# Optimization experiments

Measured on AMD Instinct MI355X. Metric: run time of the kernel, lower is better.

The kernel has to match this reference:

```python
import jax, jax.numpy as jnp
import numpy as np

B, S, E = 256, 512, 512
H = 512            # hidden_dim[0]
SUB = 512          # subreddit_embedding
TFIDF = 799
HDIMS = [256, 128] # hidden_dim[1:]


def _lin(key, fan_in, fan_out):
    kw, kb = jax.random.split(key)
    s = 1.0 / np.sqrt(fan_in)
    w = jax.random.uniform(kw, (fan_in, fan_out), jnp.float32, -s, s)
    b = jax.random.uniform(kb, (fan_out,), jnp.float32, -s, s)
    return w, b


def setup_inputs() -> dict:
    key = jax.random.key(0)
    ks = jax.random.split(key, 12)
    x = jax.random.normal(ks[0], (B, S, E), jnp.float32)
    ts = jax.random.uniform(ks[1], (B, S), jnp.float32)
    tfidf = jax.random.uniform(ks[2], (B, TFIDF), jnp.float32)
    W_all_w, W_all_b = _lin(ks[3], H, 4 * H)
    U_all_w, U_all_b = _lin(ks[4], E, 4 * H)
    W_d_w, W_d_b = _lin(ks[5], H, H)
    fc_tfidf_w, fc_tfidf_b = _lin(ks[6], TFIDF, SUB)
    l1_w, l1_b = _lin(ks[7], H + SUB, HDIMS[0])
    l2_w, l2_b = _lin(ks[8], HDIMS[0], HDIMS[1])
    lo_w, lo_b = _lin(ks[9], HDIMS[1], 2)
    return dict(historic_features=x, timestamp=ts, tf_idf_vector=tfidf,
                W_all_w=W_all_w, W_all_b=W_all_b, U_all_w=U_all_w, U_all_b=U_all_b,
                W_d_w=W_d_w, W_d_b=W_d_b, fc_tfidf_w=fc_tfidf_w, fc_tfidf_b=fc_tfidf_b,
                l1_w=l1_w, l1_b=l1_b, l2_w=l2_w, l2_b=l2_b, lo_w=lo_w, lo_b=lo_b)


def _time_lstm(x, ts, W_all_w, W_all_b, U_all_w, U_all_b, W_d_w, W_d_b):
    # Precompute input projections for all steps at once: [B,S,4H]
    u_all = jnp.einsum('bse,eh->bsh', x, U_all_w) + U_all_b

    def step(carry, xs):
        h, c = carry
        u_t, t_t = xs  # [B,4H], [B]
        c_s1 = jnp.tanh(c @ W_d_w + W_d_b)
        c_adj = (c - c_s1) + c_s1 * t_t[:, None]
        outs = h @ W_all_w + W_all_b + u_t
        f, i, o, c_tmp = jnp.split(jax.nn.sigmoid(outs), 4, axis=1)
        c_new = f * c_adj + i * c_tmp
        h_new = o * jnp.tanh(c_new)
        return (h_new, c_new), h_new

    h0 = jnp.zeros((x.shape[0], H), x.dtype)
    c0 = jnp.zeros((x.shape[0], H), x.dtype)
    (_, _), hs = jax.lax.scan(step, (h0, c0),
                              (jnp.swapaxes(u_all, 0, 1), jnp.swapaxes(ts, 0, 1)))
    return jnp.swapaxes(hs, 0, 1)  # [B,S,H]


def reference(historic_features, timestamp, tf_idf_vector,
              W_all_w, W_all_b, U_all_w, U_all_b, W_d_w, W_d_b,
              fc_tfidf_w, fc_tfidf_b, l1_w, l1_b, l2_w, l2_b, lo_w, lo_b):
    outputs = _time_lstm(historic_features, timestamp,
                         W_all_w, W_all_b, U_all_w, U_all_b, W_d_w, W_d_b)
    outputs = jnp.mean(outputs, axis=1)  # [B,H]
    sub = jax.nn.relu(tf_idf_vector @ fc_tfidf_w + fc_tfidf_b)  # [B,SUB]
    x = jnp.concatenate([sub, outputs], axis=1)  # [B, SUB+H]
    # dropout is identity in eval mode
    x = jax.nn.relu(x @ l1_w + l1_b)
    x = jax.nn.relu(x @ l2_w + l2_b)
    return x @ lo_w + lo_b  # [B,2]
```

## Files before the change

kernel.cpp:

```cpp
#include <hip/hip_runtime.h>
#include <hip/hip_cooperative_groups.h>

namespace cg = cooperative_groups;

#define BB 256
#define SS 512
#define EE 512
#define HH 512
#define G4 2048
#define NTF 799

typedef __attribute__((ext_vector_type(8))) short bf16x8;
typedef __attribute__((ext_vector_type(4))) float f32x4;

__device__ __forceinline__ float my_sig(float v) { return 1.0f / (1.0f + __expf(-v)); }
__device__ __forceinline__ float my_tanh(float v) { float e = __expf(2.0f * v); return 1.0f - 2.0f / (e + 1.0f); }

__device__ __forceinline__ unsigned short f2bf(float f) {
    unsigned u = __builtin_bit_cast(unsigned, f);
    u = (u + 0x7FFFu + ((u >> 16) & 1u)) >> 16;
    return (unsigned short)u;
}
__device__ __forceinline__ float bf2f(unsigned short h) {
    unsigned u = ((unsigned)h) << 16;
    return __builtin_bit_cast(float, u);
}
__device__ __forceinline__ unsigned packsplit(float f) {
    unsigned short hi = f2bf(f);
    unsigned short lo = f2bf(f - bf2f(hi));
    return ((unsigned)hi << 16) | (unsigned)lo;
}
__device__ __forceinline__ bf16x8 unhi(uint4 a, uint4 b) {
    union { unsigned u[4]; bf16x8 v; } r;
    r.u[0] = __builtin_amdgcn_perm(a.y, a.x, 0x07060302u);
    r.u[1] = __builtin_amdgcn_perm(a.w, a.z, 0x07060302u);
    r.u[2] = __builtin_amdgcn_perm(b.y, b.x, 0x07060302u);
    r.u[3] = __builtin_amdgcn_perm(b.w, b.z, 0x07060302u);
    return r.v;
}
__device__ __forceinline__ bf16x8 unlo(uint4 a, uint4 b) {
    union { unsigned u[4]; bf16x8 v; } r;
    r.u[0] = __builtin_amdgcn_perm(a.y, a.x, 0x05040100u);
    r.u[1] = __builtin_amdgcn_perm(a.w, a.z, 0x05040100u);
    r.u[2] = __builtin_amdgcn_perm(b.y, b.x, 0x05040100u);
    r.u[3] = __builtin_amdgcn_perm(b.w, b.z, 0x05040100u);
    return r.v;
}

__device__ __forceinline__ void ld4_sc1(uint4& d, const unsigned* p) {
    asm volatile("global_load_dwordx4 %0, %1, off sc0 sc1" : "=v"(d) : "v"(p));
}
__device__ __forceinline__ void ld4_nt(uint4& d, const uint4* p) {
    asm volatile("global_load_dwordx4 %0, %1, off nt" : "=v"(d) : "v"(p));
}
__device__ __forceinline__ void st_devu(unsigned* p, unsigned v) {
    __hip_atomic_store(p, v, __ATOMIC_RELAXED, __HIP_MEMORY_SCOPE_AGENT);
}
__device__ __forceinline__ unsigned ld_devu(const unsigned* p) {
    return __hip_atomic_load(p, __ATOMIC_RELAXED, __HIP_MEMORY_SCOPE_AGENT);
}

__global__ void __launch_bounds__(256)
prep_split(const float* __restrict__ Wall, const float* __restrict__ Uall,
           const float* __restrict__ Wd,
           unsigned short* __restrict__ B1, unsigned short* __restrict__ B2)
{
    const int t = blockIdx.x * 256 + threadIdx.x;
    if (t < 262144) {
        const int lane = t & 63, wc = (t >> 6) & 3, kc = (t >> 8) & 31, cgi = t >> 13;
        const int kb = ((kc & 15) << 5) + ((lane >> 4) << 3);
        const int col = (wc << 9) + (cgi << 4) + (lane & 15);
        const float* src = (kc < 16) ? Wall : Uall;
        bf16x8 vh, vl;
#pragma unroll
        for (int j = 0; j < 8; ++j) {
            float f = src[(size_t)(kb + j) * G4 + col];
            unsigned short h16 = f2bf(f);
            vh[j] = (short)h16;
            vl[j] = (short)f2bf(f - bf2f(h16));
        }
        const int g = t >> 6;
        *(bf16x8*)(B1 + ((size_t)(g * 2 + 0) * 64 + lane) * 8) = vh;
        *(bf16x8*)(B1 + ((size_t)(g * 2 + 1) * 64 + lane) * 8) = vl;
    } else if (t < 262144 + 32768) {
        const int u = t - 262144;
        const int lane = u & 63, kch = (u >> 6) & 15, cgi = u >> 10;
        const int kb = (kch << 5) + ((lane >> 4) << 3);
        const int col = (cgi << 4) + (lane & 15);
        bf16x8 vh, vl;
#pragma unroll
        for (int j = 0; j < 8; ++j) {
            float f = Wd[(size_t)(kb + j) * HH + col];
            unsigned short h16 = f2bf(f);
            vh[j] = (short)h16;
            vl[j] = (short)f2bf(f - bf2f(h16));
        }
        const int g = u >> 6;
        *(bf16x8*)(B2 + ((size_t)(g * 2 + 0) * 64 + lane) * 8) = vh;
        *(bf16x8*)(B2 + ((size_t)(g * 2 + 1) * 64 + lane) * 8) = vl;
    }
}

__global__ void __launch_bounds__(256)
prep_pack(const float* __restrict__ x, unsigned* __restrict__ xp)
{
    const size_t i = (size_t)blockIdx.x * 256 + threadIdx.x;
    float4 v = ((const float4*)x)[i];
    uint4 p;
    p.x = packsplit(v.x); p.y = packsplit(v.y);
    p.z = packsplit(v.z); p.w = packsplit(v.w);
    ((uint4*)xp)[i] = p;
}

#define B1FRAG(kcv, wcv, term) (*(const bf16x8*)(B1 +                          \
    ((size_t)(((cgi * 32 + (kcv)) * 4 + (wcv)) * 2 + (term)) * 64 + lane) * 8))
#define B2FRAG(kchv, term) (*(const bf16x8*)(B2 +                              \
    ((size_t)((cgi * 16 + (kchv)) * 2 + (term)) * 64 + lane) * 8))

#define GPIDX(row, slot, col)                                                  \
    ((row) * 256 + (slot) * 64 + ((col) ^ (((((row) & 3) ^ (((row) >> 2) & 3))) << 4)))

__global__ void __launch_bounds__(512) __attribute__((amdgpu_waves_per_eu(2)))
lstm_persistent(const float* __restrict__ x, const unsigned* __restrict__ xp,
                const int use_xp, const float* __restrict__ ts,
                const float* __restrict__ ball, const float* __restrict__ bu,
                const float* __restrict__ bd,
                const unsigned short* __restrict__ B1,
                const unsigned short* __restrict__ B2,
                unsigned* __restrict__ h2a, unsigned* __restrict__ h2b,
                unsigned* __restrict__ c2a, unsigned* __restrict__ c2b,
                float* __restrict__ hsum, float* __restrict__ tsT,
                unsigned* __restrict__ barv)
{
    cg::grid_group grid = cg::this_grid();
    const int tid = threadIdx.x;
    const int bid = blockIdx.x;
    const int gtid = (bid << 9) + tid;

    for (int i = gtid; i < BB * HH; i += 131072) { h2a[i] = 0u; c2a[i] = 0u; }
    for (int i = gtid; i < BB * SS; i += 131072) {
        int b = i >> 9, s = i & 511;
        tsT[s * BB + b] = ts[i];
    }
    if (gtid < 1024) barv[gtid] = 0u;
    grid.sync();

    const int xcd = bid & 7, tt = bid >> 3;
    const int cgi = (xcd << 2) | (tt & 3);
    const int rg  = tt >> 2;
    const int r0  = rg << 5;
    const int m0  = cgi << 4;

    const int wid = tid >> 6, lane = tid & 63;
    const int lrow = lane & 15, lk8 = lane >> 4;
    const int kq = wid & 3, ch = wid >> 2;
    const int srow = tid >> 4, scb = tid & 15;
    const int rl = srow, mj = scb;

    __shared__ __align__(16) unsigned R1[32 * 512];
    __shared__ __align__(16) unsigned R2[32 * 512];
    uint4* R1v = (uint4*)R1;
    uint4* R2v = (uint4*)R2;
    float* gp  = (float*)R2;
    float* gp2 = (float*)(R2 + 8192);

    unsigned* arr = barv;
    const int myline = rg << 6;

    bf16x8 wfh[4][2], wfl[4][2], d2h[2], d2l[2];
#pragma unroll
    for (int q = 0; q < 4; ++q)
#pragma unroll
        for (int wcl = 0; wcl < 2; ++wcl) {
            wfh[q][wcl] = B1FRAG((kq << 2) + q, (ch << 1) + wcl, 0);
            wfl[q][wcl] = B1FRAG((kq << 2) + q, (ch << 1) + wcl, 1);
        }
#pragma unroll
    for (int e = 0; e < 2; ++e) {
        d2h[e] = B2FRAG((wid << 1) + e, 0);
        d2l[e] = B2FRAG((wid << 1) + e, 1);
    }

    float bias4[4];
#pragma unroll
    for (int k = 0; k < 4; ++k)
        bias4[k] = ball[(k << 9) + m0 + mj] + bu[(k << 9) + m0 + mj];
    const float bias2v = bd[m0 + mj];

    float creg = 0.f, hsreg = 0.f;

#pragma unroll 1
    for (int s = 0; s < SS; ++s) {
        const unsigned* h2p = (s & 1) ? h2b : h2a;
        const unsigned* c2p = (s & 1) ? c2b : c2a;
        unsigned* h2n = (s & 1) ? h2a : h2b;
        unsigned* c2n = (s & 1) ? c2a : c2b;

        __syncthreads();
        if (use_xp) {
            const uint4* xpp = (const uint4*)(xp + (size_t)(r0 + srow) * (SS * EE)
                                              + (size_t)s * EE);
            uint4 xv[8];
#pragma unroll
            for (int j = 0; j < 8; ++j) ld4_nt(xv[j], xpp + (scb + (j << 4)));
            asm volatile("s_waitcnt vmcnt(0)" ::: "memory");
            __builtin_amdgcn_sched_barrier(0);
#pragma unroll
            for (int j = 0; j < 8; ++j) {
                const int ci = scb + (j << 4);
                R1v[srow * 128 + (ci ^ (srow & 7))] = xv[j];
            }
        } else {
            const float* xfp = x + (size_t)(r0 + srow) * (SS * EE) + (size_t)s * EE;
#pragma unroll
            for (int j = 0; j < 8; ++j) {
                const int ci = scb + (j << 4);
                float4 v = *(const float4*)(xfp + (ci << 2));
                uint4 pk;
                pk.x = packsplit(v.x); pk.y = packsplit(v.y);
                pk.z = packsplit(v.z); pk.w = packsplit(v.w);
                R1v[srow * 128 + (ci ^ (srow & 7))] = pk;
            }
        }
        __syncthreads();

        f32x4 acc[2][2];
        acc[0][0] = acc[0][1] = acc[1][0] = acc[1][1] = (f32x4){0.f, 0.f, 0.f, 0.f};
        {
            bf16x8 ufh[2][2], ufl[2][2];
#pragma unroll
            for (int wcl = 0; wcl < 2; ++wcl) {
                ufh[0][wcl] = B1FRAG(16 + (kq << 2), (ch << 1) + wcl, 0);
                ufl[0][wcl] = B1FRAG(16 + (kq << 2), (ch << 1) + wcl, 1);
            }
#pragma unroll
            for (int q = 0; q < 4; ++q) {
                const int cur = q & 1, nxt = cur ^ 1;
                if (q < 3) {
#pragma unroll
                    for (int wcl = 0; wcl < 2; ++wcl) {
                        ufh[nxt][wcl] = B1FRAG(16 + (kq << 2) + q + 1, (ch << 1) + wcl, 0);
                        ufl[nxt][wcl] = B1FRAG(16 + (kq << 2) + q + 1, (ch << 1) + wcl, 1);
                    }
                }
                const int kcp = (kq << 2) + q;
#pragma unroll
                for (int wr = 0; wr < 2; ++wr) {
                    const int row_ = (wr << 4) | lrow;
                    const int cb_  = (kcp << 3) + (lk8 << 1);
                    uint4 qa = R1v[row_ * 128 + (cb_ ^ (row_ & 7))];
                    uint4 qb = R1v[row_ * 128 + ((cb_ + 1) ^ (row_ & 7))];
                    bf16x8 ah = unhi(qa, qb), al = unlo(qa, qb);
#pragma unroll
                    for (int wcl = 0; wcl < 2; ++wcl) {
                        acc[wr][wcl] = __builtin_amdgcn_mfma_f32_16x16x32_bf16(ah, ufh[cur][wcl], acc[wr][wcl], 0, 0, 0);
                        acc[wr][wcl] = __builtin_amdgcn_mfma_f32_16x16x32_bf16(ah, ufl[cur][wcl], acc[wr][wcl], 0, 0, 0);
                        acc[wr][wcl] = __builtin_amdgcn_mfma_f32_16x16x32_bf16(al, ufh[cur][wcl], acc[wr][wcl], 0, 0, 0);
                    }
                }
            }
        }

        if (tid == 0) {
            const unsigned tgt = 32u * (unsigned)s;
            while (ld_devu(&arr[myline]) < tgt)
                __builtin_amdgcn_s_sleep(4);
        }
        __syncthreads();
        asm volatile("" ::: "memory");

        {
            const unsigned* hp = h2p + (r0 + srow) * HH;
            const unsigned* cp = c2p + (r0 + srow) * HH;
            uint4 hv[8], cv[8];
#pragma unroll
            for (int j = 0; j < 8; ++j) ld4_sc1(hv[j], hp + ((scb + (j << 4)) << 2));
#pragma unroll
            for (int j = 0; j < 8; ++j) ld4_sc1(cv[j], cp + ((scb + (j << 4)) << 2));
            asm volatile("s_waitcnt vmcnt(8)" ::: "memory");
            __builtin_amdgcn_sched_barrier(0);
#pragma unroll
            for (int j = 0; j < 8; ++j) {
                const int ci = scb + (j << 4);
                R2v[srow * 128 + (ci ^ (srow & 7))] = hv[j];
            }
            asm volatile("s_waitcnt vmcnt(0)" ::: "memory");
            __builtin_amdgcn_sched_barrier(0);
#pragma unroll
            for (int j = 0; j < 8; ++j) {
                const int ci = scb + (j << 4);
                R1v[srow * 128 + (ci ^ (srow & 7))] = cv[j];
            }
        }
        __syncthreads();

#pragma unroll
        for (int q = 0; q < 4; ++q) {
            const int kcp = (kq << 2) + q;
#pragma unroll
            for (int wr = 0; wr < 2; ++wr) {
                const int row_ = (wr << 4) | lrow;
                const int cb_  = (kcp << 3) + (lk8 << 1);
                uint4 qa = R2v[row_ * 128 + (cb_ ^ (row_ & 7))];
                uint4 qb = R2v[row_ * 128 + ((cb_ + 1) ^ (row_ & 7))];
                bf16x8 ah = unhi(qa, qb), al = unlo(qa, qb);
#pragma unroll
                for (int wcl = 0; wcl < 2; ++wcl) {
                    acc[wr][wcl] = __builtin_amdgcn_mfma_f32_16x16x32_bf16(ah, wfh[q][wcl], acc[wr][wcl], 0, 0, 0);
                    acc[wr][wcl] = __builtin_amdgcn_mfma_f32_16x16x32_bf16(ah, wfl[q][wcl], acc[wr][wcl], 0, 0, 0);
                    acc[wr][wcl] = __builtin_amdgcn_mfma_f32_16x16x32_bf16(al, wfh[q][wcl], acc[wr][wcl], 0, 0, 0);
                }
            }
        }
        f32x4 acc2[2];
        acc2[0] = (f32x4){0.f, 0.f, 0.f, 0.f};
        acc2[1] = (f32x4){0.f, 0.f, 0.f, 0.f};
#pragma unroll
        for (int e = 0; e < 2; ++e) {
            const int kch = (wid << 1) + e;
#pragma unroll
            for (int wr = 0; wr < 2; ++wr) {
                const int row_ = (wr << 4) | lrow;
                const int cb_  = (kch << 3) + (lk8 << 1);
                uint4 qa = R1v[row_ * 128 + (cb_ ^ (row_ & 7))];
                uint4 qb = R1v[row_ * 128 + ((cb_ + 1) ^ (row_ & 7))];
                bf16x8 ah = unhi(qa, qb), al = unlo(qa, qb);
                acc2[wr] = __builtin_amdgcn_mfma_f32_16x16x32_bf16(ah, d2h[e], acc2[wr], 0, 0, 0);
                acc2[wr] = __builtin_amdgcn_mfma_f32_16x16x32_bf16(ah, d2l[e], acc2[wr], 0, 0, 0);
                acc2[wr] = __builtin_amdgcn_mfma_f32_16x16x32_bf16(al, d2h[e], acc2[wr], 0, 0, 0);
            }
        }
        __syncthreads();

#pragma unroll
        for (int wr = 0; wr < 2; ++wr)
#pragma unroll
            for (int wcl = 0; wcl < 2; ++wcl)
#pragma unroll
                for (int i = 0; i < 4; ++i)
                    gp[GPIDX((wr << 4) + (lk8 << 2) + i, kq, ((ch << 1) + wcl) * 16 + lrow)] = acc[wr][wcl][i];
#pragma unroll
        for (int wr = 0; wr < 2; ++wr)
#pragma unroll
            for (int i = 0; i < 4; ++i)
                gp2[((wr << 4) + (lk8 << 2) + i) * 132 + (wid << 4) + lrow] = acc2[wr][i];
        __syncthreads();

        {
            float gv[4];
#pragma unroll
            for (int k = 0; k < 4; ++k) {
                float sacc = bias4[k];
#pragma unroll
                for (int p = 0; p < 4; ++p)
                    sacc += gp[GPIDX(rl, p, (k << 4) + mj)];
                gv[k] = my_sig(sacc);
            }
            float sacc2 = bias2v;
#pragma unroll
            for (int p = 0; p < 8; ++p)
                sacc2 += gp2[rl * 132 + (p << 4) + mj];
            const float cs1v = my_tanh(sacc2);
            const float tv = tsT[s * BB + r0 + rl];
            const float cadj = creg + cs1v * (tv - 1.0f);
            const float cnew = gv[0] * cadj + gv[1] * gv[3];
            const float hnew = gv[2] * my_tanh(cnew);
            creg = cnew; hsreg += hnew;
            const int gidx = (r0 + rl) * HH + m0 + mj;
            st_devu(&c2n[gidx], packsplit(cnew));
            st_devu(&h2n[gidx], packsplit(hnew));
        }

        asm volatile("s_waitcnt vmcnt(0)" ::: "memory");
        __syncthreads();
        if (tid == 0)
            __hip_atomic_fetch_add(&arr[myline], 1u, __ATOMIC_RELAXED,
                                   __HIP_MEMORY_SCOPE_AGENT);
    }

    hsum[(r0 + rl) * HH + m0 + mj] = hsreg;
}

__global__ void __launch_bounds__(256)
tail_kernel(const float* __restrict__ tfidf, const float* __restrict__ hsum,
            const float* __restrict__ fcw, const float* __restrict__ fcb,
            const float* __restrict__ l1w, const float* __restrict__ l1b,
            const float* __restrict__ l2w, const float* __restrict__ l2b,
            const float* __restrict__ low, const float* __restrict__ lob,
            float* __restrict__ out)
{
    const int row = blockIdx.x;
    const int t = threadIdx.x;
    __shared__ float tf[800];
    __shared__ float xrow[1024];
    __shared__ float y1[256];
    __shared__ float y2[128];

    for (int k = t; k < NTF; k += 256) tf[k] = tfidf[row * NTF + k];
    __syncthreads();

    for (int n = t; n < 512; n += 256) {
        float acc = fcb[n];
        for (int k = 0; k < NTF; ++k) acc += tf[k] * fcw[k * 512 + n];
        xrow[n] = fmaxf(acc, 0.f);
    }
    for (int n = t; n < 512; n += 256)
        xrow[512 + n] = hsum[row * HH + n] * (1.0f / 512.0f);
    __syncthreads();

    {
        float acc = l1b[t];
        for (int k = 0; k < 1024; ++k) acc += xrow[k] * l1w[k * 256 + t];
        y1[t] = fmaxf(acc, 0.f);
    }
    __syncthreads();
    if (t < 128) {
        float acc = l2b[t];
        for (int k = 0; k < 256; ++k) acc += y1[k] * l2w[k * 128 + t];
        y2[t] = fmaxf(acc, 0.f);
    }
    __syncthreads();
    if (t < 2) {
        float acc = lob[t];
        for (int k = 0; k < 128; ++k) acc += y2[k] * low[k * 2 + t];
        out[row * 2 + t] = acc;
    }
}

extern "C" void kernel_launch(void* const* d_in, const int* in_sizes, int n_in,
                              void* d_out, int out_size, void* d_ws, size_t ws_size,
                              hipStream_t stream)
{
    const float* x     = (const float*)d_in[0];
    const float* ts    = (const float*)d_in[1];
    const float* tfidf = (const float*)d_in[2];
    const float* Wall  = (const float*)d_in[3];
    const float* ball  = (const float*)d_in[4];
    const float* Uall  = (const float*)d_in[5];
    const float* bu    = (const float*)d_in[6];
    const float* Wd    = (const float*)d_in[7];
    const float* bd    = (const float*)d_in[8];
    const float* fcw   = (const float*)d_in[9];
    const float* fcb   = (const float*)d_in[10];
    const float* l1w   = (const float*)d_in[11];
    const float* l1b   = (const float*)d_in[12];
    const float* l2w   = (const float*)d_in[13];
    const float* l2b   = (const float*)d_in[14];
    const float* low   = (const float*)d_in[15];
    const float* lob   = (const float*)d_in[16];
    float* out = (float*)d_out;

    unsigned* wsu = (unsigned*)d_ws;
    unsigned* h2a = wsu;
    unsigned* h2b = h2a + BB * HH;
    unsigned* c2a = h2b + BB * HH;
    unsigned* c2b = c2a + BB * HH;
    float* hs  = (float*)(c2b + BB * HH);
    float* tsT = hs + BB * HH;
    unsigned* barv = (unsigned*)(tsT + BB * SS);
    unsigned short* B1 = (unsigned short*)(barv + 1024);
    unsigned short* B2 = B1 + (size_t)32 * 32 * 4 * 2 * 64 * 8;
    unsigned* xpk = (unsigned*)(B2 + (size_t)32 * 16 * 2 * 64 * 8);
    const size_t need = ((char*)(xpk + (size_t)BB * SS * EE)) - (char*)d_ws;
    const int use_xp = (ws_size >= need) ? 1 : 0;

    prep_split<<<1152, 256, 0, stream>>>(Wall, Uall, Wd, B1, B2);
    if (use_xp)
        prep_pack<<<65536, 256, 0, stream>>>(x, xpk);

    void* args[] = { (void*)&x, (void*)&xpk, (void*)&use_xp, (void*)&ts,
                     (void*)&ball, (void*)&bu, (void*)&bd,
                     (void*)&B1, (void*)&B2,
                     (void*)&h2a, (void*)&h2b, (void*)&c2a, (void*)&c2b,
                     (void*)&hs, (void*)&tsT, (void*)&barv };
    hipLaunchCooperativeKernel((void*)lstm_persistent, dim3(256), dim3(512), args, 0, stream);

    tail_kernel<<<256, 256, 0, stream>>>(tfidf, hs, fcw, fcb, l1w, l1b, l2w, l2b,
                                         low, lob, out);
}
```

Measured before the change: 4.940 ms.

## Load x, h and c fragments directly from global into registers, bypassing LDS staging

Per-step x, h and c tiles used to be staged through shared memory with cooperative loads and block barriers, then re-read as MFMA fragments. Each wave now loads its own MFMA A-fragments straight from global memory into registers, double-buffered with vmcnt waits so loads overlap the MFMAs. This removes LDS round-trips and several __syncthreads per timestep and shrinks the LDS footprint. In exchange, global accesses are less coalesced and some data is re-fetched by multiple waves.

```diff
diff --git a/kernel.cpp b/kernel.cpp
--- a/kernel.cpp
+++ b/kernel.cpp
@@ -12,6 +12,8 @@
 
 typedef __attribute__((ext_vector_type(8))) short bf16x8;
 typedef __attribute__((ext_vector_type(4))) float f32x4;
+
+#define MF(a, b, c) __builtin_amdgcn_mfma_f32_16x16x32_bf16((a), (b), (c), 0, 0, 0)
 
 __device__ __forceinline__ float my_sig(float v) { return 1.0f / (1.0f + __expf(-v)); }
 __device__ __forceinline__ float my_tanh(float v) { float e = __expf(2.0f * v); return 1.0f - 2.0f / (e + 1.0f); }
@@ -50,7 +52,7 @@
 __device__ __forceinline__ void ld4_sc1(uint4& d, const unsigned* p) {
     asm volatile("global_load_dwordx4 %0, %1, off sc0 sc1" : "=v"(d) : "v"(p));
 }
-__device__ __forceinline__ void ld4_nt(uint4& d, const uint4* p) {
+__device__ __forceinline__ void ld4_nt(uint4& d, const unsigned* p) {
     asm volatile("global_load_dwordx4 %0, %1, off nt" : "=v"(d) : "v"(p));
 }
 __device__ __forceinline__ void st_devu(unsigned* p, unsigned v) {
@@ -59,6 +61,10 @@
 __device__ __forceinline__ unsigned ld_devu(const unsigned* p) {
     return __hip_atomic_load(p, __ATOMIC_RELAXED, __HIP_MEMORY_SCOPE_AGENT);
 }
+
+#define VMW(N)                                                                 \
+    asm volatile("s_waitcnt vmcnt(" #N ")" ::: "memory");                      \
+    __builtin_amdgcn_sched_barrier(0)
 
 __global__ void __launch_bounds__(256)
 prep_split(const float* __restrict__ Wall, const float* __restrict__ Uall,
@@ -102,14 +108,14 @@
 }
 
 __global__ void __launch_bounds__(256)
-prep_pack(const float* __restrict__ x, unsigned* __restrict__ xp)
+prep_pack(const float* __restrict__ x, unsigned* __restrict__ xpk)
 {
     const size_t i = (size_t)blockIdx.x * 256 + threadIdx.x;
     float4 v = ((const float4*)x)[i];
     uint4 p;
     p.x = packsplit(v.x); p.y = packsplit(v.y);
     p.z = packsplit(v.z); p.w = packsplit(v.w);
-    ((uint4*)xp)[i] = p;
+    ((uint4*)xpk)[i] = p;
 }
 
 #define B1FRAG(kcv, wcv, term) (*(const bf16x8*)(B1 +                          \
@@ -154,13 +160,9 @@
     const int wid = tid >> 6, lane = tid & 63;
     const int lrow = lane & 15, lk8 = lane >> 4;
     const int kq = wid & 3, ch = wid >> 2;
-    const int srow = tid >> 4, scb = tid & 15;
-    const int rl = srow, mj = scb;
-
-    __shared__ __align__(16) unsigned R1[32 * 512];
-    __shared__ __align__(16) unsigned R2[32 * 512];
-    uint4* R1v = (uint4*)R1;
-    uint4* R2v = (uint4*)R2;
+    const int rl = tid >> 4, mj = tid & 15;
+
+    __shared__ __align__(16) unsigned R2[12416];
     float* gp  = (float*)R2;
     float* gp2 = (float*)(R2 + 8192);
 
@@ -186,6 +188,13 @@
     for (int k = 0; k < 4; ++k)
         bias4[k] = ball[(k << 9) + m0 + mj] + bu[(k << 9) + m0 + mj];
     const float bias2v = bd[m0 + mj];
+
+    const size_t xoff0 = (size_t)(r0 + lrow) * (SS * EE) + (kq << 7) + (lk8 << 3);
+    const size_t xoff1 = xoff0 + (size_t)16 * (SS * EE);
+    const int hoff0 = (r0 + lrow) * HH + (kq << 7) + (lk8 << 3);
+    const int hoff1 = hoff0 + 16 * HH;
+    const int coff0 = (r0 + lrow) * HH + (wid << 6) + (lk8 << 3);
+    const int coff1 = coff0 + 16 * HH;
 
     float creg = 0.f, hsreg = 0.f;
 
@@ -195,68 +204,86 @@
         const unsigned* c2p = (s & 1) ? c2b : c2a;
         unsigned* h2n = (s & 1) ? h2a : h2b;
         unsigned* c2n = (s & 1) ? c2a : c2b;
-
-        __syncthreads();
-        if (use_xp) {
-            const uint4* xpp = (const uint4*)(xp + (size_t)(r0 + srow) * (SS * EE)
-                                              + (size_t)s * EE);
-            uint4 xv[8];
-#pragma unroll
-            for (int j = 0; j < 8; ++j) ld4_nt(xv[j], xpp + (scb + (j << 4)));
-            asm volatile("s_waitcnt vmcnt(0)" ::: "memory");
-            __builtin_amdgcn_sched_barrier(0);
-#pragma unroll
-            for (int j = 0; j < 8; ++j) {
-                const int ci = scb + (j << 4);
-                R1v[srow * 128 + (ci ^ (srow & 7))] = xv[j];
-            }
-        } else {
-            const float* xfp = x + (size_t)(r0 + srow) * (SS * EE) + (size_t)s * EE;
-#pragma unroll
-            for (int j = 0; j < 8; ++j) {
-                const int ci = scb + (j << 4);
-                float4 v = *(const float4*)(xfp + (ci << 2));
-                uint4 pk;
-                pk.x = packsplit(v.x); pk.y = packsplit(v.y);
-                pk.z = packsplit(v.z); pk.w = packsplit(v.w);
-                R1v[srow * 128 + (ci ^ (srow & 7))] = pk;
-            }
-        }
-        __syncthreads();
+        const size_t sb = (size_t)s * EE;
 
         f32x4 acc[2][2];
         acc[0][0] = acc[0][1] = acc[1][0] = acc[1][1] = (f32x4){0.f, 0.f, 0.f, 0.f};
         {
+            uint4 xq[2][2][2];
             bf16x8 ufh[2][2], ufl[2][2];
 #pragma unroll
             for (int wcl = 0; wcl < 2; ++wcl) {
                 ufh[0][wcl] = B1FRAG(16 + (kq << 2), (ch << 1) + wcl, 0);
                 ufl[0][wcl] = B1FRAG(16 + (kq << 2), (ch << 1) + wcl, 1);
             }
-#pragma unroll
-            for (int q = 0; q < 4; ++q) {
-                const int cur = q & 1, nxt = cur ^ 1;
-                if (q < 3) {
-#pragma unroll
-                    for (int wcl = 0; wcl < 2; ++wcl) {
-                        ufh[nxt][wcl] = B1FRAG(16 + (kq << 2) + q + 1, (ch << 1) + wcl, 0);
-                        ufl[nxt][wcl] = B1FRAG(16 + (kq << 2) + q + 1, (ch << 1) + wcl, 1);
+
+#define PHA_Q(B, cur)                                                          \
+            { _Pragma("unroll")                                                \
+              for (int wr = 0; wr < 2; ++wr) {                                 \
+                  bf16x8 ah = unhi(xq[B][wr][0], xq[B][wr][1]);                \
+                  bf16x8 al = unlo(xq[B][wr][0], xq[B][wr][1]);                \
+                  _Pragma("unroll")                                            \
+                  for (int wcl = 0; wcl < 2; ++wcl) {                          \
+                      acc[wr][wcl] = MF(ah, ufh[cur][wcl], acc[wr][wcl]);      \
+                      acc[wr][wcl] = MF(ah, ufl[cur][wcl], acc[wr][wcl]);      \
+                      acc[wr][wcl] = MF(al, ufh[cur][wcl], acc[wr][wcl]);      \
+                  }                                                            \
+              } }
+
+            if (use_xp) {
+                const unsigned* p0 = xp + xoff0 + sb;
+                const unsigned* p1 = xp + xoff1 + sb;
+#define ISSUE_X(B, Q)                                                          \
+                ld4_nt(xq[B][0][0], p0 + ((Q) << 5));                          \
+                ld4_nt(xq[B][0][1], p0 + ((Q) << 5) + 4);                      \
+                ld4_nt(xq[B][1][0], p1 + ((Q) << 5));                          \
+                ld4_nt(xq[B][1][1], p1 + ((Q) << 5) + 4);
+                ISSUE_X(0, 0); ISSUE_X(1, 1);
+#pragma unroll
+                for (int q = 0; q < 4; ++q) {
+                    const int cur = q & 1, nxt = cur ^ 1;
+                    if (q < 3) {
+#pragma unroll
+                        for (int wcl = 0; wcl < 2; ++wcl) {
+                            ufh[nxt][wcl] = B1FRAG(16 + (kq << 2) + q + 1, (ch << 1) + wcl, 0);
+                            ufl[nxt][wcl] = B1FRAG(16 + (kq << 2) + q + 1, (ch << 1) + wcl, 1);
+                        }
+                        VMW(4);
+                    } else {
+                        VMW(0);
                     }
+                    if (q == 0) { PHA_Q(0, 0); ISSUE_X(0, 2); }
+                    else if (q == 1) { PHA_Q(1, 1); ISSUE_X(1, 3); }
+                    else if (q == 2) { PHA_Q(0, 0); }
+                    else { PHA_Q(1, 1); }
                 }
-                const int kcp = (kq << 2) + q;
-#pragma unroll
-                for (int wr = 0; wr < 2; ++wr) {
-                    const int row_ = (wr << 4) | lrow;
-                    const int cb_  = (kcp << 3) + (lk8 << 1);
-                    uint4 qa = R1v[row_ * 128 + (cb_ ^ (row_ & 7))];
-                    uint4 qb = R1v[row_ * 128 + ((cb_ + 1) ^ (row_ & 7))];
-                    bf16x8 ah = unhi(qa, qb), al = unlo(qa, qb);
-#pragma unroll
-                    for (int wcl = 0; wcl < 2; ++wcl) {
-                        acc[wr][wcl] = __builtin_amdgcn_mfma_f32_16x16x32_bf16(ah, ufh[cur][wcl], acc[wr][wcl], 0, 0, 0);
-                        acc[wr][wcl] = __builtin_amdgcn_mfma_f32_16x16x32_bf16(ah, ufl[cur][wcl], acc[wr][wcl], 0, 0, 0);
-                        acc[wr][wcl] = __builtin_amdgcn_mfma_f32_16x16x32_bf16(al, ufh[cur][wcl], acc[wr][wcl], 0, 0, 0);
+            } else {
+                const float* f0 = x + xoff0 + sb;
+                const float* f1 = x + xoff1 + sb;
+#pragma unroll
+                for (int q = 0; q < 4; ++q) {
+                    const int cur = q & 1, nxt = cur ^ 1;
+                    if (q < 3) {
+#pragma unroll
+                        for (int wcl = 0; wcl < 2; ++wcl) {
+                            ufh[nxt][wcl] = B1FRAG(16 + (kq << 2) + q + 1, (ch << 1) + wcl, 0);
+                            ufl[nxt][wcl] = B1FRAG(16 + (kq << 2) + q + 1, (ch << 1) + wcl, 1);
+                        }
                     }
+#pragma unroll
+                    for (int wr = 0; wr < 2; ++wr) {
+                        const float* fp = wr ? f1 : f0;
+                        float4 a = *(const float4*)(fp + (q << 5));
+                        float4 b = *(const float4*)(fp + (q << 5) + 4);
+                        xq[cur][wr][0] = (uint4){packsplit(a.x), packsplit(a.y),
+                                                 packsplit(a.z), packsplit(a.w)};
+                        xq[cur][wr][1] = (uint4){packsplit(b.x), packsplit(b.y),
+                                                 packsplit(b.z), packsplit(b.w)};
+                    }
+                    if (q == 0) { PHA_Q(0, 0); }
+                    else if (q == 1) { PHA_Q(1, 1); }
+                    else if (q == 2) { PHA_Q(0, 0); }
+                    else { PHA_Q(1, 1); }
                 }
             }
         }
@@ -269,69 +296,58 @@
         __syncthreads();
         asm volatile("" ::: "memory");
 
-        {
-            const unsigned* hp = h2p + (r0 + srow) * HH;
-            const unsigned* cp = c2p + (r0 + srow) * HH;
-            uint4 hv[8], cv[8];
-#pragma unroll
-            for (int j = 0; j < 8; ++j) ld4_sc1(hv[j], hp + ((scb + (j << 4)) << 2));
-#pragma unroll
-            for (int j = 0; j < 8; ++j) ld4_sc1(cv[j], cp + ((scb + (j << 4)) << 2));
-            asm volatile("s_waitcnt vmcnt(8)" ::: "memory");
-            __builtin_amdgcn_sched_barrier(0);
-#pragma unroll
-            for (int j = 0; j < 8; ++j) {
-                const int ci = scb + (j << 4);
-                R2v[srow * 128 + (ci ^ (srow & 7))] = hv[j];
-            }
-            asm volatile("s_waitcnt vmcnt(0)" ::: "memory");
-            __builtin_amdgcn_sched_barrier(0);
-#pragma unroll
-            for (int j = 0; j < 8; ++j) {
-                const int ci = scb + (j << 4);
-                R1v[srow * 128 + (ci ^ (srow & 7))] = cv[j];
-            }
-        }
-        __syncthreads();
-
-#pragma unroll
-        for (int q = 0; q < 4; ++q) {
-            const int kcp = (kq << 2) + q;
-#pragma unroll
-            for (int wr = 0; wr < 2; ++wr) {
-                const int row_ = (wr << 4) | lrow;
-                const int cb_  = (kcp << 3) + (lk8 << 1);
-                uint4 qa = R2v[row_ * 128 + (cb_ ^ (row_ & 7))];
-                uint4 qb = R2v[row_ * 128 + ((cb_ + 1) ^ (row_ & 7))];
-                bf16x8 ah = unhi(qa, qb), al = unlo(qa, qb);
-#pragma unroll
-                for (int wcl = 0; wcl < 2; ++wcl) {
-                    acc[wr][wcl] = __builtin_amdgcn_mfma_f32_16x16x32_bf16(ah, wfh[q][wcl], acc[wr][wcl], 0, 0, 0);
-                    acc[wr][wcl] = __builtin_amdgcn_mfma_f32_16x16x32_bf16(ah, wfl[q][wcl], acc[wr][wcl], 0, 0, 0);
-                    acc[wr][wcl] = __builtin_amdgcn_mfma_f32_16x16x32_bf16(al, wfh[q][wcl], acc[wr][wcl], 0, 0, 0);
-                }
-            }
-        }
         f32x4 acc2[2];
         acc2[0] = (f32x4){0.f, 0.f, 0.f, 0.f};
         acc2[1] = (f32x4){0.f, 0.f, 0.f, 0.f};
-#pragma unroll
-        for (int e = 0; e < 2; ++e) {
-            const int kch = (wid << 1) + e;
-#pragma unroll
-            for (int wr = 0; wr < 2; ++wr) {
-                const int row_ = (wr << 4) | lrow;
-                const int cb_  = (kch << 3) + (lk8 << 1);
-                uint4 qa = R1v[row_ * 128 + (cb_ ^ (row_ & 7))];
-                uint4 qb = R1v[row_ * 128 + ((cb_ + 1) ^ (row_ & 7))];
-                bf16x8 ah = unhi(qa, qb), al = unlo(qa, qb);
-                acc2[wr] = __builtin_amdgcn_mfma_f32_16x16x32_bf16(ah, d2h[e], acc2[wr], 0, 0, 0);
-                acc2[wr] = __builtin_amdgcn_mfma_f32_16x16x32_bf16(ah, d2l[e], acc2[wr], 0, 0, 0);
-                acc2[wr] = __builtin_amdgcn_mfma_f32_16x16x32_bf16(al, d2h[e], acc2[wr], 0, 0, 0);
-            }
-        }
+        {
+            uint4 hq[2][2][2], cq[2][2][2];
+            const unsigned* hp0 = h2p + hoff0;
+            const unsigned* hp1 = h2p + hoff1;
+            const unsigned* cp0 = c2p + coff0;
+            const unsigned* cp1 = c2p + coff1;
+
+#define ISSUE_H(B, Q)                                                          \
+            ld4_sc1(hq[B][0][0], hp0 + ((Q) << 5));                            \
+            ld4_sc1(hq[B][0][1], hp0 + ((Q) << 5) + 4);                        \
+            ld4_sc1(hq[B][1][0], hp1 + ((Q) << 5));                            \
+            ld4_sc1(hq[B][1][1], hp1 + ((Q) << 5) + 4);
+#define ISSUE_C(B, E)                                                          \
+            ld4_sc1(cq[B][0][0], cp0 + ((E) << 5));                            \
+            ld4_sc1(cq[B][0][1], cp0 + ((E) << 5) + 4);                        \
+            ld4_sc1(cq[B][1][0], cp1 + ((E) << 5));                            \
+            ld4_sc1(cq[B][1][1], cp1 + ((E) << 5) + 4);
+#define PHB_Q(B, q)                                                            \
+            { _Pragma("unroll")                                                \
+              for (int wr = 0; wr < 2; ++wr) {                                 \
+                  bf16x8 ah = unhi(hq[B][wr][0], hq[B][wr][1]);                \
+                  bf16x8 al = unlo(hq[B][wr][0], hq[B][wr][1]);                \
+                  _Pragma("unroll")                                            \
+                  for (int wcl = 0; wcl < 2; ++wcl) {                          \
+                      acc[wr][wcl] = MF(ah, wfh[q][wcl], acc[wr][wcl]);        \
+                      acc[wr][wcl] = MF(ah, wfl[q][wcl], acc[wr][wcl]);        \
+                      acc[wr][wcl] = MF(al, wfh[q][wcl], acc[wr][wcl]);        \
+                  }                                                            \
+              } }
+#define G2_E(B, e)                                                             \
+            { _Pragma("unroll")                                                \
+              for (int wr = 0; wr < 2; ++wr) {                                 \
+                  bf16x8 ah = unhi(cq[B][wr][0], cq[B][wr][1]);                \
+                  bf16x8 al = unlo(cq[B][wr][0], cq[B][wr][1]);                \
+                  acc2[wr] = MF(ah, d2h[e], acc2[wr]);                         \
+                  acc2[wr] = MF(ah, d2l[e], acc2[wr]);                         \
+                  acc2[wr] = MF(al, d2h[e], acc2[wr]);                         \
+              } }
+
+            ISSUE_H(0, 0); ISSUE_H(1, 1);
+            VMW(4); PHB_Q(0, 0); ISSUE_H(0, 2);
+            VMW(4); PHB_Q(1, 1); ISSUE_H(1, 3);
+            VMW(4); PHB_Q(0, 2); ISSUE_C(0, 0); ISSUE_C(1, 1);
+            VMW(8); PHB_Q(1, 3);
+            VMW(4); G2_E(0, 0);
+            VMW(0); G2_E(1, 1);
+        }
+
         __syncthreads();
-
 #pragma unroll
         for (int wr = 0; wr < 2; ++wr)
 #pragma unroll
```

Result: slower. 7.407 ms (+49.9%).

## Precompute input projection U·x in separate GEMM kernel before recurrent loop

Applied to the files above, without the earlier changes.

Adds a u_gemm kernel that computes the x@U_all projection for all timesteps ahead of time and stores it in a workspace buffer of 1 GiB (256×512×2048 floats). The persistent LSTM kernel then loads four precomputed values per thread per step instead of staging x in shared memory and running the U-projection MFMAs inside the serial recurrence. This takes the input projection off the latency-critical sequential path. In exchange it costs an extra full-size write and read of the projection and needs a large workspace, and it falls back to the old path when the workspace is too small.

```diff
diff --git a/kernel.cpp b/kernel.cpp
--- a/kernel.cpp
+++ b/kernel.cpp
@@ -9,9 +9,12 @@
 #define HH 512
 #define G4 2048
 #define NTF 799
+#define U4PB (512 * 2048)
 
 typedef __attribute__((ext_vector_type(8))) short bf16x8;
 typedef __attribute__((ext_vector_type(4))) float f32x4;
+
+#define MF(a, b, c) __builtin_amdgcn_mfma_f32_16x16x32_bf16((a), (b), (c), 0, 0, 0)
 
 __device__ __forceinline__ float my_sig(float v) { return 1.0f / (1.0f + __expf(-v)); }
 __device__ __forceinline__ float my_tanh(float v) { float e = __expf(2.0f * v); return 1.0f - 2.0f / (e + 1.0f); }
@@ -50,7 +53,7 @@
 __device__ __forceinline__ void ld4_sc1(uint4& d, const unsigned* p) {
     asm volatile("global_load_dwordx4 %0, %1, off sc0 sc1" : "=v"(d) : "v"(p));
 }
-__device__ __forceinline__ void ld4_nt(uint4& d, const uint4* p) {
+__device__ __forceinline__ void ld4_nt(uint4& d, const unsigned* p) {
     asm volatile("global_load_dwordx4 %0, %1, off nt" : "=v"(d) : "v"(p));
 }
 __device__ __forceinline__ void st_devu(unsigned* p, unsigned v) {
@@ -102,14 +105,14 @@
 }
 
 __global__ void __launch_bounds__(256)
-prep_pack(const float* __restrict__ x, unsigned* __restrict__ xp)
+prep_pack(const float* __restrict__ x, unsigned* __restrict__ xpk)
 {
     const size_t i = (size_t)blockIdx.x * 256 + threadIdx.x;
     float4 v = ((const float4*)x)[i];
     uint4 p;
     p.x = packsplit(v.x); p.y = packsplit(v.y);
     p.z = packsplit(v.z); p.w = packsplit(v.w);
-    ((uint4*)xp)[i] = p;
+    ((uint4*)xpk)[i] = p;
 }
 
 #define B1FRAG(kcv, wcv, term) (*(const bf16x8*)(B1 +                          \
@@ -119,6 +122,121 @@
 
 #define GPIDX(row, slot, col)                                                  \
     ((row) * 256 + (slot) * 64 + ((col) ^ (((((row) & 3) ^ (((row) >> 2) & 3))) << 4)))
+
+__global__ void __launch_bounds__(512) __attribute__((amdgpu_waves_per_eu(4)))
+u_gemm(const float* __restrict__ x, const unsigned* __restrict__ xp,
+       const int use_xp, const unsigned short* __restrict__ B1,
+       float* __restrict__ uall)
+{
+    const int tid = threadIdx.x;
+    const int b = blockIdx.x;
+    const int bl = b >> 1;
+    const int s0 = (b & 1) << 8;
+    const int rg = bl >> 5, cgi = bl & 31;
+    const int r0 = rg << 5;
+
+    const int wid = tid >> 6, lane = tid & 63;
+    const int lrow = lane & 15, lk8 = lane >> 4;
+    const int kq = wid & 3, ch = wid >> 2;
+    const int srow = tid >> 4, scb = tid & 15;
+    const int rl = srow, mj = scb;
+
+    __shared__ __align__(16) unsigned R1[32 * 512];
+    uint4* R1v = (uint4*)R1;
+    float* gp = (float*)R1;
+
+    float* ub = uall + (size_t)bl * U4PB;
+
+#pragma unroll 1
+    for (int s = s0; s < s0 + 256; ++s) {
+        const size_t sb = (size_t)s * EE;
+        __syncthreads();
+        if (use_xp) {
+            const unsigned* xpp = xp + (size_t)(r0 + srow) * (SS * EE) + sb;
+            uint4 xv[8];
+#pragma unroll
+            for (int j = 0; j < 8; ++j) ld4_nt(xv[j], xpp + ((scb + (j << 4)) << 2));
+            asm volatile("s_waitcnt vmcnt(0)" ::: "memory");
+            __builtin_amdgcn_sched_barrier(0);
+#pragma unroll
+            for (int j = 0; j < 8; ++j) {
+                const int ci = scb + (j << 4);
+                R1v[srow * 128 + (ci ^ (srow & 7))] = xv[j];
+            }
+        } else {
+            const float* xfp = x + (size_t)(r0 + srow) * (SS * EE) + sb;
+#pragma unroll
+            for (int j = 0; j < 8; ++j) {
+                const int ci = scb + (j << 4);
+                float4 v = *(const float4*)(xfp + (ci << 2));
+                uint4 pk;
+                pk.x = packsplit(v.x); pk.y = packsplit(v.y);
+                pk.z = packsplit(v.z); pk.w = packsplit(v.w);
+                R1v[srow * 128 + (ci ^ (srow & 7))] = pk;
+            }
+        }
+        __syncthreads();
+
+        f32x4 acc[2][2];
+        acc[0][0] = acc[0][1] = acc[1][0] = acc[1][1] = (f32x4){0.f, 0.f, 0.f, 0.f};
+        {
+            bf16x8 ufh[2][2], ufl[2][2];
+#pragma unroll
+            for (int wcl = 0; wcl < 2; ++wcl) {
+                ufh[0][wcl] = B1FRAG(16 + (kq << 2), (ch << 1) + wcl, 0);
+                ufl[0][wcl] = B1FRAG(16 + (kq << 2), (ch << 1) + wcl, 1);
+            }
+#pragma unroll
+            for (int q = 0; q < 4; ++q) {
+                const int cur = q & 1, nxt = cur ^ 1;
+                if (q < 3) {
+#pragma unroll
+                    for (int wcl = 0; wcl < 2; ++wcl) {
+                        ufh[nxt][wcl] = B1FRAG(16 + (kq << 2) + q + 1, (ch << 1) + wcl, 0);
+                        ufl[nxt][wcl] = B1FRAG(16 + (kq << 2) + q + 1, (ch << 1) + wcl, 1);
+                    }
+                }
+                const int kcp = (kq << 2) + q;
+#pragma unroll
+                for (int wr = 0; wr < 2; ++wr) {
+                    const int row_ = (wr << 4) | lrow;
+                    const int cb_  = (kcp << 3) + (lk8 << 1);
+                    uint4 qa = R1v[row_ * 128 + (cb_ ^ (row_ & 7))];
+                    uint4 qb = R1v[row_ * 128 + ((cb_ + 1) ^ (row_ & 7))];
+                    bf16x8 ah = unhi(qa, qb), al = unlo(qa, qb);
+#pragma unroll
+                    for (int wcl = 0; wcl < 2; ++wcl) {
+                        acc[wr][wcl] = MF(ah, ufh[cur][wcl], acc[wr][wcl]);
+                        acc[wr][wcl] = MF(ah, ufl[cur][wcl], acc[wr][wcl]);
+                        acc[wr][wcl] = MF(al, ufh[cur][wcl], acc[wr][wcl]);
+                    }
+                }
+            }
+        }
+        __syncthreads();
+
+#pragma unroll
+        for (int wr = 0; wr < 2; ++wr)
+#pragma unroll
+            for (int wcl = 0; wcl < 2; ++wcl)
+#pragma unroll
+                for (int i = 0; i < 4; ++i)
+                    gp[GPIDX((wr << 4) + (lk8 << 2) + i, kq, ((ch << 1) + wcl) * 16 + lrow)] = acc[wr][wcl][i];
+        __syncthreads();
+
+        {
+            float* up = ub + (size_t)s * 2048 + (rl << 4) + mj;
+#pragma unroll
+            for (int k = 0; k < 4; ++k) {
+                float sacc = 0.f;
+#pragma unroll
+                for (int p = 0; p < 4; ++p)
+                    sacc += gp[GPIDX(rl, p, (k << 4) + mj)];
+                __builtin_nontemporal_store(sacc, up + (k << 9));
+            }
+        }
+    }
+}
 
 __global__ void __launch_bounds__(512) __attribute__((amdgpu_waves_per_eu(2)))
 lstm_persistent(const float* __restrict__ x, const unsigned* __restrict__ xp,
@@ -130,7 +248,8 @@
                 unsigned* __restrict__ h2a, unsigned* __restrict__ h2b,
                 unsigned* __restrict__ c2a, unsigned* __restrict__ c2b,
                 float* __restrict__ hsum, float* __restrict__ tsT,
-                unsigned* __restrict__ barv)
+                unsigned* __restrict__ barv,
+                const float* __restrict__ uall, const int use_u)
 {
     cg::grid_group grid = cg::this_grid();
     const int tid = threadIdx.x;
@@ -150,6 +269,7 @@
     const int rg  = tt >> 2;
     const int r0  = rg << 5;
     const int m0  = cgi << 4;
+    const int bl  = (rg << 5) | cgi;
 
     const int wid = tid >> 6, lane = tid & 63;
     const int lrow = lane & 15, lk8 = lane >> 4;
@@ -187,6 +307,8 @@
         bias4[k] = ball[(k << 9) + m0 + mj] + bu[(k << 9) + m0 + mj];
     const float bias2v = bd[m0 + mj];
 
+    const float* ubase = uall + (size_t)bl * U4PB + (rl << 4) + mj;
+
     float creg = 0.f, hsreg = 0.f;
 
 #pragma unroll 1
@@ -195,67 +317,76 @@
         const unsigned* c2p = (s & 1) ? c2b : c2a;
         unsigned* h2n = (s & 1) ? h2a : h2b;
         unsigned* c2n = (s & 1) ? c2a : c2b;
-
-        __syncthreads();
-        if (use_xp) {
-            const uint4* xpp = (const uint4*)(xp + (size_t)(r0 + srow) * (SS * EE)
-                                              + (size_t)s * EE);
-            uint4 xv[8];
-#pragma unroll
-            for (int j = 0; j < 8; ++j) ld4_nt(xv[j], xpp + (scb + (j << 4)));
-            asm volatile("s_waitcnt vmcnt(0)" ::: "memory");
-            __builtin_amdgcn_sched_barrier(0);
-#pragma unroll
-            for (int j = 0; j < 8; ++j) {
-                const int ci = scb + (j << 4);
-                R1v[srow * 128 + (ci ^ (srow & 7))] = xv[j];
-            }
-        } else {
-            const float* xfp = x + (size_t)(r0 + srow) * (SS * EE) + (size_t)s * EE;
-#pragma unroll
-            for (int j = 0; j < 8; ++j) {
-                const int ci = scb + (j << 4);
-                float4 v = *(const float4*)(xfp + (ci << 2));
-                uint4 pk;
-                pk.x = packsplit(v.x); pk.y = packsplit(v.y);
-                pk.z = packsplit(v.z); pk.w = packsplit(v.w);
-                R1v[srow * 128 + (ci ^ (srow & 7))] = pk;
-            }
-        }
-        __syncthreads();
-
+        const size_t sb = (size_t)s * EE;
+
+        float uv[4] = {0.f, 0.f, 0.f, 0.f};
         f32x4 acc[2][2];
         acc[0][0] = acc[0][1] = acc[1][0] = acc[1][1] = (f32x4){0.f, 0.f, 0.f, 0.f};
-        {
-            bf16x8 ufh[2][2], ufl[2][2];
-#pragma unroll
-            for (int wcl = 0; wcl < 2; ++wcl) {
-                ufh[0][wcl] = B1FRAG(16 + (kq << 2), (ch << 1) + wcl, 0);
-                ufl[0][wcl] = B1FRAG(16 + (kq << 2), (ch << 1) + wcl, 1);
-            }
-#pragma unroll
-            for (int q = 0; q < 4; ++q) {
-                const int cur = q & 1, nxt = cur ^ 1;
-                if (q < 3) {
-#pragma unroll
-                    for (int wcl = 0; wcl < 2; ++wcl) {
-                        ufh[nxt][wcl] = B1FRAG(16 + (kq << 2) + q + 1, (ch << 1) + wcl, 0);
-                        ufl[nxt][wcl] = B1FRAG(16 + (kq << 2) + q + 1, (ch << 1) + wcl, 1);
+
+        if (use_u) {
+            const float* up = ubase + (size_t)s * 2048;
+            uv[0] = __builtin_nontemporal_load(up);
+            uv[1] = __builtin_nontemporal_load(up + 512);
+            uv[2] = __builtin_nontemporal_load(up + 1024);
+            uv[3] = __builtin_nontemporal_load(up + 1536);
+        } else {
+            __syncthreads();
+            if (use_xp) {
+                const unsigned* xpp = xp + (size_t)(r0 + srow) * (SS * EE) + sb;
+                uint4 xv[8];
+#pragma unroll
+                for (int j = 0; j < 8; ++j) ld4_nt(xv[j], xpp + ((scb + (j << 4)) << 2));
+                asm volatile("s_waitcnt vmcnt(0)" ::: "memory");
+                __builtin_amdgcn_sched_barrier(0);
+#pragma unroll
+                for (int j = 0; j < 8; ++j) {
+                    const int ci = scb + (j << 4);
+                    R1v[srow * 128 + (ci ^ (srow & 7))] = xv[j];
+                }
+            } else {
+                const float* xfp = x + (size_t)(r0 + srow) * (SS * EE) + sb;
+#pragma unroll
+                for (int j = 0; j < 8; ++j) {
+                    const int ci = scb + (j << 4);
+                    float4 v = *(const float4*)(xfp + (ci << 2));
+                    uint4 pk;
+                    pk.x = packsplit(v.x); pk.y = packsplit(v.y);
+                    pk.z = packsplit(v.z); pk.w = packsplit(v.w);
+                    R1v[srow * 128 + (ci ^ (srow & 7))] = pk;
+                }
+            }
+            __syncthreads();
+            {
+                bf16x8 ufh[2][2], ufl[2][2];
+#pragma unroll
+                for (int wcl = 0; wcl < 2; ++wcl) {
+                    ufh[0][wcl] = B1FRAG(16 + (kq << 2), (ch << 1) + wcl, 0);
+                    ufl[0][wcl] = B1FRAG(16 + (kq << 2), (ch << 1) + wcl, 1);
+                }
+#pragma unroll
+                for (int q = 0; q < 4; ++q) {
+                    const int cur = q & 1, nxt = cur ^ 1;
+                    if (q < 3) {
+#pragma unroll
+                        for (int wcl = 0; wcl < 2; ++wcl) {
+                            ufh[nxt][wcl] = B1FRAG(16 + (kq << 2) + q + 1, (ch << 1) + wcl, 0);
+                            ufl[nxt][wcl] = B1FRAG(16 + (kq << 2) + q + 1, (ch << 1) + wcl, 1);
+                        }
                     }
-                }
-                const int kcp = (kq << 2) + q;
-#pragma unroll
-                for (int wr = 0; wr < 2; ++wr) {
-                    const int row_ = (wr << 4) | lrow;
-                    const int cb_  = (kcp << 3) + (lk8 << 1);
-                    uint4 qa = R1v[row_ * 128 + (cb_ ^ (row_ & 7))];
-                    uint4 qb = R1v[row_ * 128 + ((cb_ + 1) ^ (row_ & 7))];
-                    bf16x8 ah = unhi(qa, qb), al = unlo(qa, qb);
-#pragma unroll
-                    for (int wcl = 0; wcl < 2; ++wcl) {
-                        acc[wr][wcl] = __builtin_amdgcn_mfma_f32_16x16x32_bf16(ah, ufh[cur][wcl], acc[wr][wcl], 0, 0, 0);
-                        acc[wr][wcl] = __builtin_amdgcn_mfma_f32_16x16x32_bf16(ah, ufl[cur][wcl], acc[wr][wcl], 0, 0, 0);
-                        acc[wr][wcl] = __builtin_amdgcn_mfma_f32_16x16x32_bf16(al, ufh[cur][wcl], acc[wr][wcl], 0, 0, 0);
+                    const int kcp = (kq << 2) + q;
+#pragma unroll
+                    for (int wr = 0; wr < 2; ++wr) {
+                        const int row_ = (wr << 4) | lrow;
+                        const int cb_  = (kcp << 3) + (lk8 << 1);
+                        uint4 qa = R1v[row_ * 128 + (cb_ ^ (row_ & 7))];
+                        uint4 qb = R1v[row_ * 128 + ((cb_ + 1) ^ (row_ & 7))];
+                        bf16x8 ah = unhi(qa, qb), al = unlo(qa, qb);
+#pragma unroll
+                        for (int wcl = 0; wcl < 2; ++wcl) {
+                            acc[wr][wcl] = MF(ah, ufh[cur][wcl], acc[wr][wcl]);
+                            acc[wr][wcl] = MF(ah, ufl[cur][wcl], acc[wr][wcl]);
+                            acc[wr][wcl] = MF(al, ufh[cur][wcl], acc[wr][wcl]);
+                        }
                     }
                 }
             }
@@ -306,9 +437,9 @@
                 bf16x8 ah = unhi(qa, qb), al = unlo(qa, qb);
 #pragma unroll
                 for (int wcl = 0; wcl < 2; ++wcl) {
-                    acc[wr][wcl] = __builtin_amdgcn_mfma_f32_16x16x32_bf16(ah, wfh[q][wcl], acc[wr][wcl], 0, 0, 0);
-                    acc[wr][wcl] = __builtin_amdgcn_mfma_f32_16x16x32_bf16(ah, wfl[q][wcl], acc[wr][wcl], 0, 0, 0);
-                    acc[wr][wcl] = __builtin_amdgcn_mfma_f32_16x16x32_bf16(al, wfh[q][wcl], acc[wr][wcl], 0, 0, 0);
+                    acc[wr][wcl] = MF(ah, wfh[q][wcl], acc[wr][wcl]);
+                    acc[wr][wcl] = MF(ah, wfl[q][wcl], acc[wr][wcl]);
+                    acc[wr][wcl] = MF(al, wfh[q][wcl], acc[wr][wcl]);
                 }
             }
         }
@@ -325,9 +456,9 @@
                 uint4 qa = R1v[row_ * 128 + (cb_ ^ (row_ & 7))];
                 uint4 qb = R1v[row_ * 128 + ((cb_ + 1) ^ (row_ & 7))];
                 bf16x8 ah = unhi(qa, qb), al = unlo(qa, qb);
-                acc2[wr] = __builtin_amdgcn_mfma_f32_16x16x32_bf16(ah, d2h[e], acc2[wr], 0, 0, 0);
-                acc2[wr] = __builtin_amdgcn_mfma_f32_16x16x32_bf16(ah, d2l[e], acc2[wr], 0, 0, 0);
-                acc2[wr] = __builtin_amdgcn_mfma_f32_16x16x32_bf16(al, d2h[e], acc2[wr], 0, 0, 0);
+                acc2[wr] = MF(ah, d2h[e], acc2[wr]);
+                acc2[wr] = MF(ah, d2l[e], acc2[wr]);
+                acc2[wr] = MF(al, d2h[e], acc2[wr]);
             }
         }
         __syncthreads();
@@ -350,7 +481,7 @@
             float gv[4];
 #pragma unroll
             for (int k = 0; k < 4; ++k) {
-                float sacc = bias4[k];
+                float sacc = bias4[k] + uv[k];
 #pragma unroll
                 for (int p = 0; p < 4; ++p)
                     sacc += gp[GPIDX(rl, p, (k << 4) + mj)];
@@ -460,19 +591,26 @@
     unsigned* barv = (unsigned*)(tsT + BB * SS);
     unsigned short* B1 = (unsigned short*)(barv + 1024);
     unsigned short* B2 = B1 + (size_t)32 * 32 * 4 * 2 * 64 * 8;
-    unsigned* xpk = (unsigned*)(B2 + (size_t)32 * 16 * 2 * 64 * 8);
-    const size_t need = ((char*)(xpk + (size_t)BB * SS * EE)) - (char*)d_ws;
-    const int use_xp = (ws_size >= need) ? 1 : 0;
+    float* uall = (float*)(B2 + (size_t)32 * 16 * 2 * 64 * 8);
+    unsigned* xpk = (unsigned*)uall;
+
+    const size_t need_u  = ((char*)(uall + (size_t)256 * U4PB)) - (char*)d_ws;
+    const size_t need_xp = ((char*)(xpk + (size_t)BB * SS * EE)) - (char*)d_ws;
+    const int use_u  = (ws_size >= need_u) ? 1 : 0;
+    const int use_xp = (!use_u && ws_size >= need_xp) ? 1 : 0;
 
     prep_split<<<1152, 256, 0, stream>>>(Wall, Uall, Wd, B1, B2);
-    if (use_xp)
+    if (use_u)
+        u_gemm<<<512, 512, 0, stream>>>(x, xpk, 0, B1, uall);
+    else if (use_xp)
         prep_pack<<<65536, 256, 0, stream>>>(x, xpk);
 
     void* args[] = { (void*)&x, (void*)&xpk, (void*)&use_xp, (void*)&ts,
                      (void*)&ball, (void*)&bu, (void*)&bd,
                      (void*)&B1, (void*)&B2,
                      (void*)&h2a, (void*)&h2b, (void*)&c2a, (void*)&c2b,
-                     (void*)&hs, (void*)&tsT, (void*)&barv };
+                     (void*)&hs, (void*)&tsT, (void*)&barv,
+                     (void*)&uall, (void*)&use_u };
     hipLaunchCooperativeKernel((void*)lstm_persistent, dim3(256), dim3(512), args, 0, stream);
 
     tail_kernel<<<256, 256, 0, stream>>>(tfidf, hs, fcw, fcb, l1w, l1b, l2w, l2b,
```

Result: slower. 6.332 ms (+28.2%).
